# Kernel optimization log

Measured on AMD Instinct MI355X. Metric: run time of the kernel, lower is better.

## Reference

```python
import jax, jax.numpy as jnp
import numpy as np

N_MEL = 80
PRENET = 256
ATT_RNN = 1024
DEC_RNN = 1024
ENC = 512
ATT_DIM = 128
LOC_F = 32
LOC_K = 31


def lstm_cell(x, h, c, wih, whh, bih, bhh):
    # torch LSTMCell gate order: i, f, g, o
    gates = x @ wih.T + bih + h @ whh.T + bhh
    i, f, g, o = jnp.split(gates, 4, axis=-1)
    c_new = jax.nn.sigmoid(f) * c + jax.nn.sigmoid(i) * jnp.tanh(g)
    h_new = jax.nn.sigmoid(o) * jnp.tanh(c_new)
    return h_new, c_new


def setup_inputs() -> dict:
    key = jax.random.key(0)
    ks = jax.random.split(key, 20)
    B, T_IN, T_OUT = 64, 200, 400

    def w(k, shape, fan_in):
        return (jax.random.normal(k, shape, jnp.float32) / np.float32(np.sqrt(fan_in)))

    return {
        "memory": jax.random.normal(ks[0], (B, T_IN, ENC), jnp.float32),
        "decoder_inputs": jax.random.normal(ks[1], (B, N_MEL, T_OUT), jnp.float32),
        "memory_lengths": jax.random.randint(ks[2], (B,), T_IN // 2, T_IN + 1),
        "w_prenet1": w(ks[3], (PRENET, N_MEL), N_MEL),
        "w_prenet2": w(ks[4], (PRENET, PRENET), PRENET),
        "wih_att": w(ks[5], (4 * ATT_RNN, PRENET + ENC), PRENET + ENC),
        "whh_att": w(ks[6], (4 * ATT_RNN, ATT_RNN), ATT_RNN),
        "bih_att": jnp.zeros((4 * ATT_RNN,), jnp.float32),
        "bhh_att": jnp.zeros((4 * ATT_RNN,), jnp.float32),
        "wq": w(ks[7], (ATT_DIM, ATT_RNN), ATT_RNN),
        "wmem": w(ks[8], (ATT_DIM, ENC), ENC),
        "wv": w(ks[9], (1, ATT_DIM), ATT_DIM),
        "wconv": w(ks[10], (LOC_F, 2, LOC_K), 2 * LOC_K),
        "wloc": w(ks[11], (ATT_DIM, LOC_F), LOC_F),
        "wih_dec": w(ks[12], (4 * DEC_RNN, ATT_RNN + ENC), ATT_RNN + ENC),
        "whh_dec": w(ks[13], (4 * DEC_RNN, DEC_RNN), DEC_RNN),
        "bih_dec": jnp.zeros((4 * DEC_RNN,), jnp.float32),
        "bhh_dec": jnp.zeros((4 * DEC_RNN,), jnp.float32),
        "wproj": w(ks[14], (N_MEL, DEC_RNN + ENC), DEC_RNN + ENC),
        "bproj": jnp.zeros((N_MEL,), jnp.float32),
        "wgate": w(ks[15], (1, DEC_RNN + ENC), DEC_RNN + ENC),
        "bgate": jnp.zeros((1,), jnp.float32),
    }


def reference(memory, decoder_inputs, memory_lengths, w_prenet1, w_prenet2,
              wih_att, whh_att, bih_att, bhh_att, wq, wmem, wv, wconv, wloc,
              wih_dec, whh_dec, bih_dec, bhh_dec, wproj, bproj, wgate, bgate):
    B, T_in, _ = memory.shape
    T_out = decoder_inputs.shape[2]

    # parse_decoder_inputs: [B, n_mel, T_out] -> [T_out, B, n_mel]; prepend go frame
    dec_in = jnp.transpose(decoder_inputs, (2, 0, 1))
    dec_in = jnp.concatenate([jnp.zeros((1, B, N_MEL), dec_in.dtype), dec_in], axis=0)

    # PreNet: linear -> relu -> dropout(0.5, training=True always in source)
    dk1, dk2 = jax.random.split(jax.random.key(42))
    x = jax.nn.relu(dec_in @ w_prenet1.T)
    x = jnp.where(jax.random.bernoulli(dk1, 0.5, x.shape), x * 2.0, 0.0)
    x = jax.nn.relu(x @ w_prenet2.T)
    x = jnp.where(jax.random.bernoulli(dk2, 0.5, x.shape), x * 2.0, 0.0)
    x = x[:T_out]  # teacher-forcing inputs, one per decode step

    proc_mem = memory @ wmem.T                                   # [B, T_in, ATT_DIM]
    pad_mask = jnp.arange(T_in)[None, :] >= memory_lengths[:, None]  # True = padded

    def step(carry, x_t):
        att_h, att_c, dec_h, dec_c, aw, awc, ctx = carry
        att_h, att_c = lstm_cell(jnp.concatenate([x_t, ctx], -1), att_h, att_c,
                                 wih_att, whh_att, bih_att, bhh_att)
        # location-sensitive attention
        awcat = jnp.stack([aw, awc], axis=1)                     # [B, 2, T_in]
        loc = jax.lax.conv_general_dilated(
            awcat, wconv, (1,), [(LOC_K // 2, LOC_K // 2)],
            dimension_numbers=("NCH", "OIH", "NCH"))             # [B, LOC_F, T_in]
        proc_loc = jnp.einsum("bft,df->btd", loc, wloc)          # [B, T_in, ATT_DIM]
        pq = att_h @ wq.T                                        # [B, ATT_DIM]
        e = jnp.tanh(proc_mem + pq[:, None, :] + proc_loc) @ wv[0]  # [B, T_in]
        e = jnp.where(pad_mask, -1e9, e)
        aw_new = jax.nn.softmax(e, axis=1)
        ctx = jnp.einsum("bt,bte->be", aw_new, memory)           # [B, ENC]
        awc = awc + aw_new
        dec_h, dec_c = lstm_cell(jnp.concatenate([att_h, ctx], -1), dec_h, dec_c,
                                 wih_dec, whh_dec, bih_dec, bhh_dec)
        dha = jnp.concatenate([dec_h, ctx], axis=1)              # [B, DEC_RNN+ENC]
        mel = dha @ wproj.T + bproj                              # [B, N_MEL]
        gate = dha @ wgate.T + bgate                             # [B, 1]
        return (att_h, att_c, dec_h, dec_c, aw_new, awc, ctx), (mel, gate[:, 0], aw_new)

    z = jnp.zeros
    init = (z((B, ATT_RNN)), z((B, ATT_RNN)), z((B, DEC_RNN)), z((B, DEC_RNN)),
            z((B, T_in)), z((B, T_in)), z((B, ENC)))
    _, (mels, gates, aligns) = jax.lax.scan(step, init, x)
    mel_outputs = jnp.transpose(mels, (1, 2, 0))    # [B, n_mel, T_out]
    gate_outputs = jnp.transpose(gates, (1, 0))     # [B, T_out]
    alignments = jnp.transpose(aligns, (1, 0, 2))   # [B, T_out, T_in]
    return mel_outputs, gate_outputs, alignments
```

## Files before the change

kernel.cpp:

```cpp
#include <hip/hip_runtime.h>
#include <hip/hip_bf16.h>
#include <stdint.h>
#include <stddef.h>

#define SPLIT_MODE 0
#define BITS_MODE  0
#define KSPLIT 16

#define B_    64
#define TIN   200
#define TOUT  400
#define ENC   512
#define NMEL  80
#define PRE   256
#define RNN   1024
#define G4    4096
#define ATTD  128
#define LOCF  32
#define LOCK  31
#define MSIZE 6569984u

__host__ __device__ inline void tf2x32(uint32_t k0, uint32_t k1, uint32_t x0, uint32_t x1,
                                       uint32_t* o0, uint32_t* o1) {
  uint32_t k2 = k0 ^ k1 ^ 0x1BD11BDAu;
#define TFROT(v, r) (((v) << (r)) | ((v) >> (32 - (r))))
#define TFR(r) { x0 += x1; x1 = TFROT(x1, r); x1 ^= x0; }
  x0 += k0; x1 += k1;
  TFR(13) TFR(15) TFR(26) TFR(6)  x0 += k1; x1 += k2 + 1u;
  TFR(17) TFR(29) TFR(16) TFR(24) x0 += k2; x1 += k0 + 2u;
  TFR(13) TFR(15) TFR(26) TFR(6)  x0 += k0; x1 += k1 + 3u;
  TFR(17) TFR(29) TFR(16) TFR(24) x0 += k1; x1 += k2 + 4u;
  TFR(13) TFR(15) TFR(26) TFR(6)  x0 += k2; x1 += k0 + 5u;
  *o0 = x0; *o1 = x1;
#undef TFR
#undef TFROT
}

__device__ inline bool tf_keep(uint32_t ka, uint32_t kb, uint32_t idx) {
#if BITS_MODE == 0
  uint32_t a, b; tf2x32(ka, kb, 0u, idx, &a, &b);
  return (((a ^ b) >> 31) == 0u);
#else
  const uint32_t HALF = MSIZE / 2u;
  uint32_t a, b;
  if (idx < HALF) { tf2x32(ka, kb, idx, idx + HALF, &a, &b); return ((a >> 31) == 0u); }
  else            { tf2x32(ka, kb, idx - HALF, idx, &a, &b); return ((b >> 31) == 0u); }
#endif
}

__device__ inline float sigf(float x) { return 1.f / (1.f + __expf(-x)); }

static const size_t OFF_PM   = 0;
static const size_t OFF_XS   = OFF_PM   + (size_t)B_ * TIN * ATTD;
static const size_t OFF_HATT = OFF_XS   + (size_t)B_ * PRE;
static const size_t OFF_CATT = OFF_HATT + (size_t)B_ * RNN;
static const size_t OFF_HDEC = OFF_CATT + (size_t)B_ * RNN;
static const size_t OFF_CDEC = OFF_HDEC + (size_t)B_ * RNN;
static const size_t OFF_CTX  = OFF_CDEC + (size_t)B_ * RNN;
static const size_t OFF_AW   = OFF_CTX  + (size_t)B_ * ENC;
static const size_t OFF_AWC  = OFF_AW   + (size_t)B_ * TIN;
static const size_t OFF_PART = OFF_AWC  + (size_t)B_ * TIN;

__global__ __launch_bounds__(256) void k_init(float* s, int n) {
  int i = blockIdx.x * 256 + threadIdx.x;
  if (i < n) s[i] = 0.f;
}

__global__ __launch_bounds__(128) void k_procmem(const float* __restrict__ memory,
    const float* __restrict__ wmem, float* __restrict__ pm) {
  int b = blockIdx.x / TIN, tt = blockIdx.x % TIN;
  int d = threadIdx.x;
  __shared__ __align__(16) float m_s[ENC];
  for (int k = d; k < ENC; k += 128) m_s[k] = memory[((size_t)b * TIN + tt) * ENC + k];
  __syncthreads();
  float a = 0.f;
  const float4* w4 = (const float4*)(wmem + (size_t)d * ENC);
  const float4* m4 = (const float4*)m_s;
  #pragma unroll 8
  for (int k = 0; k < ENC / 4; ++k) {
    float4 w = w4[k], v = m4[k];
    a += w.x * v.x + w.y * v.y + w.z * v.z + w.w * v.w;
  }
  pm[((size_t)b * TIN + tt) * ATTD + d] = a;
}

#define WSTR 132
__global__ __launch_bounds__(256) void k_gates(
    const float* __restrict__ in1, int L1,
    const float* __restrict__ in2, int L2,
    const float* __restrict__ in3,
    const float* __restrict__ wih, int wihK,
    const float* __restrict__ whh,
    float* __restrict__ part, int nch) {
  int ctile = blockIdx.x;
  int ks = blockIdx.y;
  int tid = threadIdx.x;
  int cg = tid & 31, bg = tid >> 5;
  __shared__ float xin_s[64 * 68];
  __shared__ float w_s[64 * WSTR];
  float acc[8][4];
  #pragma unroll
  for (int i = 0; i < 8; ++i)
    #pragma unroll
    for (int j = 0; j < 4; ++j) acc[i][j] = 0.f;

  int c_begin = (ks * nch) / KSPLIT, c_end = ((ks + 1) * nch) / KSPLIT;
  for (int cc = c_begin; cc < c_end; ++cc) {
    int k0 = cc * 64;
    const float* src; int sl, so;
    if (k0 < L1)            { src = in1; sl = L1;   so = k0; }
    else if (k0 < L1 + L2)  { src = in2; sl = L2;   so = k0 - L1; }
    else                    { src = in3; sl = 1024; so = k0 - L1 - L2; }
    const float* wsrc; int wl, wo;
    if (k0 < wihK) { wsrc = wih; wl = wihK; wo = k0; }
    else           { wsrc = whh; wl = 1024; wo = k0 - wihK; }

    __syncthreads();
    #pragma unroll
    for (int i = 0; i < 16; ++i) {
      int idx = tid + 256 * i;
      int b = idx >> 6, kk = idx & 63;
      xin_s[kk * 68 + b] = src[(size_t)b * sl + so + kk];
    }
    #pragma unroll
    for (int i = 0; i < 8; ++i) {
      int idx = tid + 256 * i;
      int c = idx >> 4, kq = idx & 15;
      float4 w = *(const float4*)&wsrc[(size_t)(ctile * 128 + c) * wl + wo + kq * 4];
      w_s[(kq * 4 + 0) * WSTR + c] = w.x;
      w_s[(kq * 4 + 1) * WSTR + c] = w.y;
      w_s[(kq * 4 + 2) * WSTR + c] = w.z;
      w_s[(kq * 4 + 3) * WSTR + c] = w.w;
    }
    __syncthreads();
    #pragma unroll 4
    for (int kk = 0; kk < 64; ++kk) {
      float4 w  = *(const float4*)&w_s[kk * WSTR + cg * 4];
      float4 x0 = *(const float4*)&xin_s[kk * 68 + bg * 8];
      float4 x1 = *(const float4*)&xin_s[kk * 68 + bg * 8 + 4];
      float xr[8] = {x0.x, x0.y, x0.z, x0.w, x1.x, x1.y, x1.z, x1.w};
      float wr[4] = {w.x, w.y, w.z, w.w};
      #pragma unroll
      for (int i = 0; i < 8; ++i)
        #pragma unroll
        for (int j = 0; j < 4; ++j) acc[i][j] += xr[i] * wr[j];
    }
  }
  #pragma unroll
  for (int i = 0; i < 8; ++i) {
    float* dst = part + ((size_t)ks * B_ + (bg * 8 + i)) * G4 + ctile * 128 + cg * 4;
    *(float4*)dst = make_float4(acc[i][0], acc[i][1], acc[i][2], acc[i][3]);
  }
}

__global__ __launch_bounds__(512) void k_attention(
    const float* __restrict__ part, float* __restrict__ hatt, float* __restrict__ catt,
    float* __restrict__ aw, float* __restrict__ awc, float* __restrict__ ctx,
    const float* __restrict__ pm, const float* __restrict__ memory,
    const float* __restrict__ wq, const float* __restrict__ wv,
    const float* __restrict__ wconv, const float* __restrict__ wloc,
    const float* __restrict__ bih, const float* __restrict__ bhh,
    const int* __restrict__ memlen, float* __restrict__ out_align, int t) {
  int b = blockIdx.x, tid = threadIdx.x;
  __shared__ float h_s[RNN];
  __shared__ float aw_s[TIN], awc_s[TIN];
  __shared__ float loc_s[LOCF * TIN];
  __shared__ float pq_s[ATTD];
  __shared__ float e4_s[4 * TIN];
  __shared__ float red[512];
  __shared__ float wl_s[ATTD * LOCF];
  __shared__ float wc_s[LOCF * 2 * LOCK];

  for (int k = tid; k < ATTD * LOCF; k += 512) wl_s[k] = wloc[k];
  for (int k = tid; k < LOCF * 2 * LOCK; k += 512) wc_s[k] = wconv[k];

  #pragma unroll
  for (int r = 0; r < 2; ++r) {
    int j = tid + 512 * r;
    float ig = bih[j] + bhh[j];
    float fg = bih[RNN + j] + bhh[RNN + j];
    float gg = bih[2 * RNN + j] + bhh[2 * RNN + j];
    float og = bih[3 * RNN + j] + bhh[3 * RNN + j];
    #pragma unroll
    for (int ks = 0; ks < KSPLIT; ++ks) {
      const float* pr = part + ((size_t)ks * B_ + b) * G4;
      ig += pr[j]; fg += pr[RNN + j]; gg += pr[2 * RNN + j]; og += pr[3 * RNN + j];
    }
    float c = sigf(fg) * catt[(size_t)b * RNN + j] + sigf(ig) * tanhf(gg);
    float h = sigf(og) * tanhf(c);
    catt[(size_t)b * RNN + j] = c;
    hatt[(size_t)b * RNN + j] = h;
    h_s[j] = h;
  }
  for (int k = tid; k < TIN; k += 512) { aw_s[k] = aw[(size_t)b * TIN + k]; awc_s[k] = awc[(size_t)b * TIN + k]; }
  __syncthreads();

  {
    int d = tid & 127, hf = tid >> 7;
    float a = 0.f;
    const float* wr = wq + (size_t)d * RNN + hf * 256;
    const float* hr = h_s + hf * 256;
    #pragma unroll 8
    for (int k = 0; k < 256; ++k) a += hr[k] * wr[k];
    red[tid] = a;
  }
  __syncthreads();
  if (tid < ATTD) pq_s[tid] = red[tid] + red[tid + 128] + red[tid + 256] + red[tid + 384];

  for (int task = tid; task < LOCF * TIN; task += 512) {
    int f = task / TIN, tt = task % TIN;
    float a = 0.f;
    #pragma unroll
    for (int k = 0; k < LOCK; ++k) {
      int s = tt + k - 15;
      if (s >= 0 && s < TIN)
        a += aw_s[s] * wc_s[f * (2 * LOCK) + k] + awc_s[s] * wc_s[f * (2 * LOCK) + LOCK + k];
    }
    loc_s[task] = a;
  }
  __syncthreads();

  for (int task = tid; task < 4 * TIN; task += 512) {
    int hf = task / TIN, tt = task - hf * TIN;
    float acc = 0.f;
    const float* pmr = pm + ((size_t)b * TIN + tt) * ATTD;
    #pragma unroll 4
    for (int d = hf * 32; d < hf * 32 + 32; ++d) {
      float pl = 0.f;
      #pragma unroll
      for (int f = 0; f < LOCF; ++f) pl += loc_s[f * TIN + tt] * wl_s[d * LOCF + f];
      acc += tanhf(pmr[d] + pq_s[d] + pl) * wv[d];
    }
    e4_s[task] = acc;
  }
  __syncthreads();

  int len = memlen[b];
  float ev = -3.0e38f;
  if (tid < TIN)
    ev = (tid < len) ? (e4_s[tid] + e4_s[TIN + tid] + e4_s[2 * TIN + tid] + e4_s[3 * TIN + tid])
                     : -1.0e9f;
  red[tid] = ev;
  __syncthreads();
  for (int s = 256; s > 0; s >>= 1) { if (tid < s) red[tid] = fmaxf(red[tid], red[tid + s]); __syncthreads(); }
  float m = red[0];
  __syncthreads();
  float p = (tid < TIN) ? __expf(ev - m) : 0.f;
  red[tid] = p;
  __syncthreads();
  for (int s = 256; s > 0; s >>= 1) { if (tid < s) red[tid] += red[tid + s]; __syncthreads(); }
  float inv = 1.f / red[0];
  __syncthreads();
  if (tid < TIN) {
    float a = p * inv;
    aw[(size_t)b * TIN + tid] = a;
    awc[(size_t)b * TIN + tid] = awc_s[tid] + a;
    out_align[((size_t)b * TOUT + t) * TIN + tid] = a;
    aw_s[tid] = a;
  }
  __syncthreads();

  {
    float a = 0.f;
    const float* mr = memory + (size_t)b * TIN * ENC + tid;
    #pragma unroll 8
    for (int tt = 0; tt < TIN; ++tt) a += aw_s[tt] * mr[(size_t)tt * ENC];
    ctx[(size_t)b * ENC + tid] = a;
  }
}

__global__ __launch_bounds__(512) void k_outphase(
    const float* __restrict__ part, const float* __restrict__ ctx,
    float* __restrict__ hdec, float* __restrict__ cdec,
    const float* __restrict__ bih, const float* __restrict__ bhh,
    const float* __restrict__ wproj, const float* __restrict__ bproj,
    const float* __restrict__ wgate, const float* __restrict__ bgate,
    float* __restrict__ out,
    const float* __restrict__ dec, const float* __restrict__ w1,
    const float* __restrict__ w2, float* __restrict__ xs,
    uint32_t k1a, uint32_t k1b, uint32_t k2a, uint32_t k2b, int t) {
  int b = blockIdx.x, tid = threadIdx.x;
  __shared__ float dha_s[RNN + ENC];
  __shared__ float red[512];
  __shared__ __align__(16) float in_s[NMEL];
  __shared__ __align__(16) float h2_s[PRE];
  #pragma unroll
  for (int r = 0; r < 2; ++r) {
    int j = tid + 512 * r;
    float ig = bih[j] + bhh[j];
    float fg = bih[RNN + j] + bhh[RNN + j];
    float gg = bih[2 * RNN + j] + bhh[2 * RNN + j];
    float og = bih[3 * RNN + j] + bhh[3 * RNN + j];
    #pragma unroll
    for (int ks = 0; ks < KSPLIT; ++ks) {
      const float* pr = part + ((size_t)ks * B_ + b) * G4;
      ig += pr[j]; fg += pr[RNN + j]; gg += pr[2 * RNN + j]; og += pr[3 * RNN + j];
    }
    float c = sigf(fg) * cdec[(size_t)b * RNN + j] + sigf(ig) * tanhf(gg);
    float h = sigf(og) * tanhf(c);
    cdec[(size_t)b * RNN + j] = c;
    hdec[(size_t)b * RNN + j] = h;
    dha_s[j] = h;
  }
  for (int k = tid; k < ENC; k += 512) dha_s[RNN + k] = ctx[(size_t)b * ENC + k];
  if (t + 1 < TOUT && tid < NMEL)
    in_s[tid] = dec[((size_t)b * NMEL + tid) * TOUT + t];
  __syncthreads();
  float mp = 0.f;
  if (tid < 4 * NMEL) {
    int m = tid % NMEL, hf = tid / NMEL;
    const float* wr = wproj + (size_t)m * (RNN + ENC) + hf * 384;
    const float* dr = dha_s + hf * 384;
    #pragma unroll 8
    for (int k = 0; k < 384; ++k) mp += dr[k] * wr[k];
  }
  red[tid] = mp;
  __syncthreads();
  if (tid < NMEL) {
    float mel = red[tid] + red[tid + NMEL] + red[tid + 2 * NMEL] + red[tid + 3 * NMEL] + bproj[tid];
    out[((size_t)b * NMEL + tid) * TOUT + t] = mel;
  }
  __syncthreads();
  float g = 0.f;
  for (int k = tid; k < RNN + ENC; k += 512) g += dha_s[k] * wgate[k];
  red[tid] = g;
  __syncthreads();
  for (int s = 256; s > 0; s >>= 1) { if (tid < s) red[tid] += red[tid + s]; __syncthreads(); }
  if (tid == 0) out[(size_t)2048000 + (size_t)b * TOUT + t] = red[0] + bgate[0];

  if (t + 1 < TOUT) {
    int tn = t + 1;
    if (tid < PRE) {
      float a = 0.f;
      const float4* w14 = (const float4*)(w1 + (size_t)tid * NMEL);
      const float4* i4  = (const float4*)in_s;
      #pragma unroll
      for (int k = 0; k < NMEL / 4; ++k) {
        float4 w = w14[k], v = i4[k];
        a += w.x * v.x + w.y * v.y + w.z * v.z + w.w * v.w;
      }
      a = fmaxf(a, 0.f);
      uint32_t idx = (uint32_t)((tn * 64 + b) * 256 + tid);
      a = tf_keep(k1a, k1b, idx) ? a * 2.f : 0.f;
      h2_s[tid] = a;
    }
    __syncthreads();
    if (tid < PRE) {
      float a2 = 0.f;
      const float4* w24 = (const float4*)(w2 + (size_t)tid * PRE);
      const float4* h4  = (const float4*)h2_s;
      #pragma unroll 8
      for (int k = 0; k < PRE / 4; ++k) {
        float4 w = w24[k], v = h4[k];
        a2 += w.x * v.x + w.y * v.y + w.z * v.z + w.w * v.w;
      }
      a2 = fmaxf(a2, 0.f);
      uint32_t idx = (uint32_t)((tn * 64 + b) * 256 + tid);
      a2 = tf_keep(k2a, k2b, idx) ? a2 * 2.f : 0.f;
      xs[((size_t)b << 8) + tid] = a2;
    }
  }
}

extern "C" void kernel_launch(void* const* d_in, const int* in_sizes, int n_in,
                              void* d_out, int out_size, void* d_ws, size_t ws_size,
                              hipStream_t stream) {
  (void)in_sizes; (void)n_in; (void)out_size; (void)ws_size;
  const float* memory  = (const float*)d_in[0];
  const float* dec     = (const float*)d_in[1];
  const int*   mlen    = (const int*)d_in[2];
  const float* w1      = (const float*)d_in[3];
  const float* w2      = (const float*)d_in[4];
  const float* wih_att = (const float*)d_in[5];
  const float* whh_att = (const float*)d_in[6];
  const float* bih_att = (const float*)d_in[7];
  const float* bhh_att = (const float*)d_in[8];
  const float* wq      = (const float*)d_in[9];
  const float* wmem    = (const float*)d_in[10];
  const float* wv      = (const float*)d_in[11];
  const float* wconv   = (const float*)d_in[12];
  const float* wloc    = (const float*)d_in[13];
  const float* wih_dec = (const float*)d_in[14];
  const float* whh_dec = (const float*)d_in[15];
  const float* bih_dec = (const float*)d_in[16];
  const float* bhh_dec = (const float*)d_in[17];
  const float* wproj   = (const float*)d_in[18];
  const float* bproj   = (const float*)d_in[19];
  const float* wgate   = (const float*)d_in[20];
  const float* bgate   = (const float*)d_in[21];
  float* out = (float*)d_out;
  float* ws  = (float*)d_ws;

  uint32_t dk1a, dk1b, dk2a, dk2b;
#if SPLIT_MODE == 0
  tf2x32(0u, 42u, 0u, 0u, &dk1a, &dk1b);
  tf2x32(0u, 42u, 0u, 1u, &dk2a, &dk2b);
#else
  uint32_t a0, b0, a1, b1;
  tf2x32(0u, 42u, 0u, 2u, &a0, &b0);
  tf2x32(0u, 42u, 1u, 3u, &a1, &b1);
  dk1a = a0; dk1b = a1; dk2a = b0; dk2b = b1;
#endif

  float* pm   = ws + OFF_PM;
  float* xs   = ws + OFF_XS;
  float* hatt = ws + OFF_HATT; float* catt = ws + OFF_CATT;
  float* hdec = ws + OFF_HDEC; float* cdec = ws + OFF_CDEC;
  float* ctxp = ws + OFF_CTX;
  float* aw   = ws + OFF_AW;   float* awc  = ws + OFF_AWC;
  float* part = ws + OFF_PART;

  int nstate = B_ * (PRE + 4 * RNN + ENC + 2 * TIN);
  k_init<<<(nstate + 255) / 256, 256, 0, stream>>>(xs, nstate);
  k_procmem<<<B_ * TIN, 128, 0, stream>>>(memory, wmem, pm);

  float* out_align = out + 2073600;
  for (int t = 0; t < TOUT; ++t) {
    k_gates<<<dim3(32, KSPLIT), 256, 0, stream>>>(xs, PRE, ctxp, ENC, hatt,
                                                  wih_att, PRE + ENC, whh_att,
                                                  part, 28);
    k_attention<<<B_, 512, 0, stream>>>(part, hatt, catt, aw, awc, ctxp, pm, memory,
                                        wq, wv, wconv, wloc, bih_att, bhh_att,
                                        mlen, out_align, t);
    k_gates<<<dim3(32, KSPLIT), 256, 0, stream>>>(hatt, RNN, ctxp, ENC, hdec,
                                                  wih_dec, RNN + ENC, whh_dec,
                                                  part, 40);
    k_outphase<<<B_, 512, 0, stream>>>(part, ctxp, hdec, cdec, bih_dec, bhh_dec,
                                       wproj, bproj, wgate, bgate, out,
                                       dec, w1, w2, xs, dk1a, dk1b, dk2a, dk2b, t);
  }
}
```

Measured before the change: 68.45 ms.

## Fuse per-timestep kernels into one persistent cooperative kernel with grid syncs

Replaces the four kernel launches per decoder step (1600 in total) with a single cooperative kernel. It loops over all timesteps and separates the gate GEMM, attention, second gate GEMM and output phases with grid-wide syncs. The gate GEMM is remapped to 256 blocks of 512 threads with a K-split of 8 and smaller per-thread tiles. Shared memory becomes a union covering every phase. The aim is to remove launch gaps and per-launch overhead. In exchange, attention and output phases still use only 64 of 256 blocks, grid barriers carry their own cost, and the GEMM tiling changes.

```diff
diff --git a/kernel.cpp b/kernel.cpp
--- a/kernel.cpp
+++ b/kernel.cpp
@@ -1,11 +1,12 @@
 #include <hip/hip_runtime.h>
 #include <hip/hip_bf16.h>
+#include <hip/hip_cooperative_groups.h>
 #include <stdint.h>
 #include <stddef.h>
 
 #define SPLIT_MODE 0
 #define BITS_MODE  0
-#define KSPLIT 16
+#define KSPLIT 8
 
 #define B_    64
 #define TIN   200
@@ -19,6 +20,9 @@
 #define LOCF  32
 #define LOCK  31
 #define MSIZE 6569984u
+#define WSTR  132
+
+namespace cg = cooperative_groups;
 
 __host__ __device__ inline void tf2x32(uint32_t k0, uint32_t k1, uint32_t x0, uint32_t x1,
                                        uint32_t* o0, uint32_t* o1) {
@@ -61,6 +65,27 @@
 static const size_t OFF_AWC  = OFF_AW   + (size_t)B_ * TIN;
 static const size_t OFF_PART = OFF_AWC  + (size_t)B_ * TIN;
 
+union SM {
+  struct { float xin[64 * 68]; float w[64 * WSTR]; } g;
+  struct {
+    float h[RNN]; float awp[TIN]; float awcp[TIN]; float loc[LOCF * TIN];
+    float pq[ATTD]; float e4[4 * TIN]; float red[512];
+    float wl[ATTD * LOCF]; float wc[LOCF * 2 * LOCK];
+  } a;
+  struct { float dha[RNN + ENC]; float red[512]; float inm[NMEL]; float h2[PRE]; } o;
+};
+
+struct Params {
+  const float *memory, *dec, *w1, *w2;
+  const float *wih_att, *whh_att, *bih_att, *bhh_att;
+  const float *wq, *wv, *wconv, *wloc;
+  const float *wih_dec, *whh_dec, *bih_dec, *bhh_dec;
+  const float *wproj, *bproj, *wgate, *bgate;
+  const int* mlen;
+  float *out, *out_align, *pm, *xs, *hatt, *catt, *hdec, *cdec, *ctx, *aw, *awc, *part;
+  uint32_t k1a, k1b, k2a, k2b;
+};
+
 __global__ __launch_bounds__(256) void k_init(float* s, int n) {
   int i = blockIdx.x * 256 + threadIdx.x;
   if (i < n) s[i] = 0.f;
@@ -84,27 +109,18 @@
   pm[((size_t)b * TIN + tt) * ATTD + d] = a;
 }
 
-#define WSTR 132
-__global__ __launch_bounds__(256) void k_gates(
-    const float* __restrict__ in1, int L1,
-    const float* __restrict__ in2, int L2,
-    const float* __restrict__ in3,
-    const float* __restrict__ wih, int wihK,
-    const float* __restrict__ whh,
-    float* __restrict__ part, int nch) {
-  int ctile = blockIdx.x;
-  int ks = blockIdx.y;
-  int tid = threadIdx.x;
+__device__ void gates_phase(SM* sm, const float* in1, int L1, const float* in2, int L2,
+    const float* in3, const float* wih, int wihK, const float* whh,
+    float* part, int nch, int bid, int tid) {
+  int ctile = bid & 31, ks = bid >> 5;
   int cg = tid & 31, bg = tid >> 5;
-  __shared__ float xin_s[64 * 68];
-  __shared__ float w_s[64 * WSTR];
-  float acc[8][4];
+  float acc[4][4];
   #pragma unroll
-  for (int i = 0; i < 8; ++i)
+  for (int i = 0; i < 4; ++i)
     #pragma unroll
     for (int j = 0; j < 4; ++j) acc[i][j] = 0.f;
 
-  int c_begin = (ks * nch) / KSPLIT, c_end = ((ks + 1) * nch) / KSPLIT;
+  int c_begin = (ks * nch) >> 3, c_end = ((ks + 1) * nch) >> 3;
   for (int cc = c_begin; cc < c_end; ++cc) {
     int k0 = cc * 64;
     const float* src; int sl, so;
@@ -117,95 +133,81 @@
 
     __syncthreads();
     #pragma unroll
-    for (int i = 0; i < 16; ++i) {
-      int idx = tid + 256 * i;
+    for (int i = 0; i < 8; ++i) {
+      int idx = tid + 512 * i;
       int b = idx >> 6, kk = idx & 63;
-      xin_s[kk * 68 + b] = src[(size_t)b * sl + so + kk];
-    }
-    #pragma unroll
-    for (int i = 0; i < 8; ++i) {
-      int idx = tid + 256 * i;
+      sm->g.xin[kk * 68 + b] = src[(size_t)b * sl + so + kk];
+    }
+    #pragma unroll
+    for (int i = 0; i < 4; ++i) {
+      int idx = tid + 512 * i;
       int c = idx >> 4, kq = idx & 15;
       float4 w = *(const float4*)&wsrc[(size_t)(ctile * 128 + c) * wl + wo + kq * 4];
-      w_s[(kq * 4 + 0) * WSTR + c] = w.x;
-      w_s[(kq * 4 + 1) * WSTR + c] = w.y;
-      w_s[(kq * 4 + 2) * WSTR + c] = w.z;
-      w_s[(kq * 4 + 3) * WSTR + c] = w.w;
+      sm->g.w[(kq * 4 + 0) * WSTR + c] = w.x;
+      sm->g.w[(kq * 4 + 1) * WSTR + c] = w.y;
+      sm->g.w[(kq * 4 + 2) * WSTR + c] = w.z;
+      sm->g.w[(kq * 4 + 3) * WSTR + c] = w.w;
     }
     __syncthreads();
     #pragma unroll 4
     for (int kk = 0; kk < 64; ++kk) {
-      float4 w  = *(const float4*)&w_s[kk * WSTR + cg * 4];
-      float4 x0 = *(const float4*)&xin_s[kk * 68 + bg * 8];
-      float4 x1 = *(const float4*)&xin_s[kk * 68 + bg * 8 + 4];
-      float xr[8] = {x0.x, x0.y, x0.z, x0.w, x1.x, x1.y, x1.z, x1.w};
+      float4 w = *(const float4*)&sm->g.w[kk * WSTR + cg * 4];
+      float4 x = *(const float4*)&sm->g.xin[kk * 68 + bg * 4];
+      float xr[4] = {x.x, x.y, x.z, x.w};
       float wr[4] = {w.x, w.y, w.z, w.w};
       #pragma unroll
-      for (int i = 0; i < 8; ++i)
+      for (int i = 0; i < 4; ++i)
         #pragma unroll
         for (int j = 0; j < 4; ++j) acc[i][j] += xr[i] * wr[j];
     }
   }
   #pragma unroll
-  for (int i = 0; i < 8; ++i) {
-    float* dst = part + ((size_t)ks * B_ + (bg * 8 + i)) * G4 + ctile * 128 + cg * 4;
+  for (int i = 0; i < 4; ++i) {
+    float* dst = part + ((size_t)ks * B_ + (bg * 4 + i)) * G4 + ctile * 128 + cg * 4;
     *(float4*)dst = make_float4(acc[i][0], acc[i][1], acc[i][2], acc[i][3]);
   }
 }
 
-__global__ __launch_bounds__(512) void k_attention(
-    const float* __restrict__ part, float* __restrict__ hatt, float* __restrict__ catt,
-    float* __restrict__ aw, float* __restrict__ awc, float* __restrict__ ctx,
-    const float* __restrict__ pm, const float* __restrict__ memory,
-    const float* __restrict__ wq, const float* __restrict__ wv,
-    const float* __restrict__ wconv, const float* __restrict__ wloc,
-    const float* __restrict__ bih, const float* __restrict__ bhh,
-    const int* __restrict__ memlen, float* __restrict__ out_align, int t) {
-  int b = blockIdx.x, tid = threadIdx.x;
-  __shared__ float h_s[RNN];
-  __shared__ float aw_s[TIN], awc_s[TIN];
-  __shared__ float loc_s[LOCF * TIN];
-  __shared__ float pq_s[ATTD];
-  __shared__ float e4_s[4 * TIN];
-  __shared__ float red[512];
-  __shared__ float wl_s[ATTD * LOCF];
-  __shared__ float wc_s[LOCF * 2 * LOCK];
-
-  for (int k = tid; k < ATTD * LOCF; k += 512) wl_s[k] = wloc[k];
-  for (int k = tid; k < LOCF * 2 * LOCK; k += 512) wc_s[k] = wconv[k];
+__device__ void attention_phase(SM* sm, const Params& p, int b, int tid, int t) {
+  for (int k = tid; k < ATTD * LOCF; k += 512) sm->a.wl[k] = p.wloc[k];
+  for (int k = tid; k < LOCF * 2 * LOCK; k += 512) sm->a.wc[k] = p.wconv[k];
 
   #pragma unroll
   for (int r = 0; r < 2; ++r) {
     int j = tid + 512 * r;
-    float ig = bih[j] + bhh[j];
-    float fg = bih[RNN + j] + bhh[RNN + j];
-    float gg = bih[2 * RNN + j] + bhh[2 * RNN + j];
-    float og = bih[3 * RNN + j] + bhh[3 * RNN + j];
+    float ig = p.bih_att[j] + p.bhh_att[j];
+    float fg = p.bih_att[RNN + j] + p.bhh_att[RNN + j];
+    float gg = p.bih_att[2 * RNN + j] + p.bhh_att[2 * RNN + j];
+    float og = p.bih_att[3 * RNN + j] + p.bhh_att[3 * RNN + j];
     #pragma unroll
     for (int ks = 0; ks < KSPLIT; ++ks) {
-      const float* pr = part + ((size_t)ks * B_ + b) * G4;
+      const float* pr = p.part + ((size_t)ks * B_ + b) * G4;
       ig += pr[j]; fg += pr[RNN + j]; gg += pr[2 * RNN + j]; og += pr[3 * RNN + j];
     }
-    float c = sigf(fg) * catt[(size_t)b * RNN + j] + sigf(ig) * tanhf(gg);
+    float c = sigf(fg) * p.catt[(size_t)b * RNN + j] + sigf(ig) * tanhf(gg);
     float h = sigf(og) * tanhf(c);
-    catt[(size_t)b * RNN + j] = c;
-    hatt[(size_t)b * RNN + j] = h;
-    h_s[j] = h;
-  }
-  for (int k = tid; k < TIN; k += 512) { aw_s[k] = aw[(size_t)b * TIN + k]; awc_s[k] = awc[(size_t)b * TIN + k]; }
+    p.catt[(size_t)b * RNN + j] = c;
+    p.hatt[(size_t)b * RNN + j] = h;
+    sm->a.h[j] = h;
+  }
+  for (int k = tid; k < TIN; k += 512) {
+    sm->a.awp[k] = p.aw[(size_t)b * TIN + k];
+    sm->a.awcp[k] = p.awc[(size_t)b * TIN + k];
+  }
   __syncthreads();
 
   {
     int d = tid & 127, hf = tid >> 7;
     float a = 0.f;
-    const float* wr = wq + (size_t)d * RNN + hf * 256;
-    const float* hr = h_s + hf * 256;
+    const float* wr = p.wq + (size_t)d * RNN + hf * 256;
+    const float* hr = sm->a.h + hf * 256;
     #pragma unroll 8
     for (int k = 0; k < 256; ++k) a += hr[k] * wr[k];
-    red[tid] = a;
-  }
-  __syncthreads();
-  if (tid < ATTD) pq_s[tid] = red[tid] + red[tid + 128] + red[tid + 256] + red[tid + 384];
+    sm->a.red[tid] = a;
+  }
+  __syncthreads();
+  if (tid < ATTD)
+    sm->a.pq[tid] = sm->a.red[tid] + sm->a.red[tid + 128] + sm->a.red[tid + 256] + sm->a.red[tid + 384];
 
   for (int task = tid; task < LOCF * TIN; task += 512) {
     int f = task / TIN, tt = task % TIN;
@@ -214,126 +216,123 @@
     for (int k = 0; k < LOCK; ++k) {
       int s = tt + k - 15;
       if (s >= 0 && s < TIN)
-        a += aw_s[s] * wc_s[f * (2 * LOCK) + k] + awc_s[s] * wc_s[f * (2 * LOCK) + LOCK + k];
-    }
-    loc_s[task] = a;
+        a += sm->a.awp[s] * sm->a.wc[f * (2 * LOCK) + k] + sm->a.awcp[s] * sm->a.wc[f * (2 * LOCK) + LOCK + k];
+    }
+    sm->a.loc[task] = a;
   }
   __syncthreads();
 
   for (int task = tid; task < 4 * TIN; task += 512) {
     int hf = task / TIN, tt = task - hf * TIN;
     float acc = 0.f;
-    const float* pmr = pm + ((size_t)b * TIN + tt) * ATTD;
+    const float* pmr = p.pm + ((size_t)b * TIN + tt) * ATTD;
     #pragma unroll 4
     for (int d = hf * 32; d < hf * 32 + 32; ++d) {
       float pl = 0.f;
       #pragma unroll
-      for (int f = 0; f < LOCF; ++f) pl += loc_s[f * TIN + tt] * wl_s[d * LOCF + f];
-      acc += tanhf(pmr[d] + pq_s[d] + pl) * wv[d];
-    }
-    e4_s[task] = acc;
-  }
-  __syncthreads();
-
-  int len = memlen[b];
+      for (int f = 0; f < LOCF; ++f) pl += sm->a.loc[f * TIN + tt] * sm->a.wl[d * LOCF + f];
+      acc += tanhf(pmr[d] + sm->a.pq[d] + pl) * p.wv[d];
+    }
+    sm->a.e4[task] = acc;
+  }
+  __syncthreads();
+
+  int len = p.mlen[b];
   float ev = -3.0e38f;
   if (tid < TIN)
-    ev = (tid < len) ? (e4_s[tid] + e4_s[TIN + tid] + e4_s[2 * TIN + tid] + e4_s[3 * TIN + tid])
+    ev = (tid < len) ? (sm->a.e4[tid] + sm->a.e4[TIN + tid] + sm->a.e4[2 * TIN + tid] + sm->a.e4[3 * TIN + tid])
                      : -1.0e9f;
-  red[tid] = ev;
-  __syncthreads();
-  for (int s = 256; s > 0; s >>= 1) { if (tid < s) red[tid] = fmaxf(red[tid], red[tid + s]); __syncthreads(); }
-  float m = red[0];
-  __syncthreads();
-  float p = (tid < TIN) ? __expf(ev - m) : 0.f;
-  red[tid] = p;
-  __syncthreads();
-  for (int s = 256; s > 0; s >>= 1) { if (tid < s) red[tid] += red[tid + s]; __syncthreads(); }
-  float inv = 1.f / red[0];
+  sm->a.red[tid] = ev;
+  __syncthreads();
+  for (int s = 256; s > 0; s >>= 1) {
+    if (tid < s) sm->a.red[tid] = fmaxf(sm->a.red[tid], sm->a.red[tid + s]);
+    __syncthreads();
+  }
+  float m = sm->a.red[0];
+  __syncthreads();
+  float pr = (tid < TIN) ? __expf(ev - m) : 0.f;
+  sm->a.red[tid] = pr;
+  __syncthreads();
+  for (int s = 256; s > 0; s >>= 1) {
+    if (tid < s) sm->a.red[tid] += sm->a.red[tid + s];
+    __syncthreads();
+  }
+  float inv = 1.f / sm->a.red[0];
   __syncthreads();
   if (tid < TIN) {
-    float a = p * inv;
-    aw[(size_t)b * TIN + tid] = a;
-    awc[(size_t)b * TIN + tid] = awc_s[tid] + a;
-    out_align[((size_t)b * TOUT + t) * TIN + tid] = a;
-    aw_s[tid] = a;
+    float a = pr * inv;
+    p.aw[(size_t)b * TIN + tid] = a;
+    p.awc[(size_t)b * TIN + tid] = sm->a.awcp[tid] + a;
+    p.out_align[((size_t)b * TOUT + t) * TIN + tid] = a;
+    sm->a.awp[tid] = a;
   }
   __syncthreads();
 
   {
     float a = 0.f;
-    const float* mr = memory + (size_t)b * TIN * ENC + tid;
+    const float* mr = p.memory + (size_t)b * TIN * ENC + tid;
     #pragma unroll 8
-    for (int tt = 0; tt < TIN; ++tt) a += aw_s[tt] * mr[(size_t)tt * ENC];
-    ctx[(size_t)b * ENC + tid] = a;
-  }
-}
-
-__global__ __launch_bounds__(512) void k_outphase(
-    const float* __restrict__ part, const float* __restrict__ ctx,
-    float* __restrict__ hdec, float* __restrict__ cdec,
-    const float* __restrict__ bih, const float* __restrict__ bhh,
-    const float* __restrict__ wproj, const float* __restrict__ bproj,
-    const float* __restrict__ wgate, const float* __restrict__ bgate,
-    float* __restrict__ out,
-    const float* __restrict__ dec, const float* __restrict__ w1,
-    const float* __restrict__ w2, float* __restrict__ xs,
-    uint32_t k1a, uint32_t k1b, uint32_t k2a, uint32_t k2b, int t) {
-  int b = blockIdx.x, tid = threadIdx.x;
-  __shared__ float dha_s[RNN + ENC];
-  __shared__ float red[512];
-  __shared__ __align__(16) float in_s[NMEL];
-  __shared__ __align__(16) float h2_s[PRE];
+    for (int tt = 0; tt < TIN; ++tt) a += sm->a.awp[tt] * mr[(size_t)tt * ENC];
+    p.ctx[(size_t)b * ENC + tid] = a;
+  }
+}
+
+__device__ void outphase_phase(SM* sm, const Params& p, int b, int tid, int t) {
   #pragma unroll
   for (int r = 0; r < 2; ++r) {
     int j = tid + 512 * r;
-    float ig = bih[j] + bhh[j];
-    float fg = bih[RNN + j] + bhh[RNN + j];
-    float gg = bih[2 * RNN + j] + bhh[2 * RNN + j];
-    float og = bih[3 * RNN + j] + bhh[3 * RNN + j];
+    float ig = p.bih_dec[j] + p.bhh_dec[j];
+    float fg = p.bih_dec[RNN + j] + p.bhh_dec[RNN + j];
+    float gg = p.bih_dec[2 * RNN + j] + p.bhh_dec[2 * RNN + j];
+    float og = p.bih_dec[3 * RNN + j] + p.bhh_dec[3 * RNN + j];
     #pragma unroll
     for (int ks = 0; ks < KSPLIT; ++ks) {
-      const float* pr = part + ((size_t)ks * B_ + b) * G4;
+      const float* pr = p.part + ((size_t)ks * B_ + b) * G4;
       ig += pr[j]; fg += pr[RNN + j]; gg += pr[2 * RNN + j]; og += pr[3 * RNN + j];
     }
-    float c = sigf(fg) * cdec[(size_t)b * RNN + j] + sigf(ig) * tanhf(gg);
+    float c = sigf(fg) * p.cdec[(size_t)b * RNN + j] + sigf(ig) * tanhf(gg);
     float h = sigf(og) * tanhf(c);
-    cdec[(size_t)b * RNN + j] = c;
-    hdec[(size_t)b * RNN + j] = h;
-    dha_s[j] = h;
-  }
-  for (int k = tid; k < ENC; k += 512) dha_s[RNN + k] = ctx[(size_t)b * ENC + k];
+    p.cdec[(size_t)b * RNN + j] = c;
+    p.hdec[(size_t)b * RNN + j] = h;
+    sm->o.dha[j] = h;
+  }
+  for (int k = tid; k < ENC; k += 512) sm->o.dha[RNN + k] = p.ctx[(size_t)b * ENC + k];
   if (t + 1 < TOUT && tid < NMEL)
-    in_s[tid] = dec[((size_t)b * NMEL + tid) * TOUT + t];
-  __syncthreads();
+    sm->o.inm[tid] = p.dec[((size_t)b * NMEL + tid) * TOUT + t];
+  __syncthreads();
+
   float mp = 0.f;
   if (tid < 4 * NMEL) {
     int m = tid % NMEL, hf = tid / NMEL;
-    const float* wr = wproj + (size_t)m * (RNN + ENC) + hf * 384;
-    const float* dr = dha_s + hf * 384;
+    const float* wr = p.wproj + (size_t)m * (RNN + ENC) + hf * 384;
+    const float* dr = sm->o.dha + hf * 384;
     #pragma unroll 8
     for (int k = 0; k < 384; ++k) mp += dr[k] * wr[k];
   }
-  red[tid] = mp;
+  sm->o.red[tid] = mp;
   __syncthreads();
   if (tid < NMEL) {
-    float mel = red[tid] + red[tid + NMEL] + red[tid + 2 * NMEL] + red[tid + 3 * NMEL] + bproj[tid];
-    out[((size_t)b * NMEL + tid) * TOUT + t] = mel;
+    float mel = sm->o.red[tid] + sm->o.red[tid + NMEL] + sm->o.red[tid + 2 * NMEL]
+              + sm->o.red[tid + 3 * NMEL] + p.bproj[tid];
+    p.out[((size_t)b * NMEL + tid) * TOUT + t] = mel;
   }
   __syncthreads();
   float g = 0.f;
-  for (int k = tid; k < RNN + ENC; k += 512) g += dha_s[k] * wgate[k];
-  red[tid] = g;
-  __syncthreads();
-  for (int s = 256; s > 0; s >>= 1) { if (tid < s) red[tid] += red[tid + s]; __syncthreads(); }
-  if (tid == 0) out[(size_t)2048000 + (size_t)b * TOUT + t] = red[0] + bgate[0];
+  for (int k = tid; k < RNN + ENC; k += 512) g += sm->o.dha[k] * p.wgate[k];
+  sm->o.red[tid] = g;
+  __syncthreads();
+  for (int s = 256; s > 0; s >>= 1) {
+    if (tid < s) sm->o.red[tid] += sm->o.red[tid + s];
+    __syncthreads();
+  }
+  if (tid == 0) p.out[(size_t)2048000 + (size_t)b * TOUT + t] = sm->o.red[0] + p.bgate[0];
 
   if (t + 1 < TOUT) {
     int tn = t + 1;
     if (tid < PRE) {
       float a = 0.f;
-      const float4* w14 = (const float4*)(w1 + (size_t)tid * NMEL);
-      const float4* i4  = (const float4*)in_s;
+      const float4* w14 = (const float4*)(p.w1 + (size_t)tid * NMEL);
+      const float4* i4  = (const float4*)sm->o.inm;
       #pragma unroll
       for (int k = 0; k < NMEL / 4; ++k) {
         float4 w = w14[k], v = i4[k];
@@ -341,14 +340,14 @@
       }
       a = fmaxf(a, 0.f);
       uint32_t idx = (uint32_t)((tn * 64 + b) * 256 + tid);
-      a = tf_keep(k1a, k1b, idx) ? a * 2.f : 0.f;
-      h2_s[tid] = a;
+      a = tf_keep(p.k1a, p.k1b, idx) ? a * 2.f : 0.f;
+      sm->o.h2[tid] = a;
     }
     __syncthreads();
     if (tid < PRE) {
       float a2 = 0.f;
-      const float4* w24 = (const float4*)(w2 + (size_t)tid * PRE);
-      const float4* h4  = (const float4*)h2_s;
+      const float4* w24 = (const float4*)(p.w2 + (size_t)tid * PRE);
+      const float4* h4  = (const float4*)sm->o.h2;
       #pragma unroll 8
       for (int k = 0; k < PRE / 4; ++k) {
         float4 w = w24[k], v = h4[k];
@@ -356,9 +355,35 @@
       }
       a2 = fmaxf(a2, 0.f);
       uint32_t idx = (uint32_t)((tn * 64 + b) * 256 + tid);
-      a2 = tf_keep(k2a, k2b, idx) ? a2 * 2.f : 0.f;
-      xs[((size_t)b << 8) + tid] = a2;
-    }
+      a2 = tf_keep(p.k2a, p.k2b, idx) ? a2 * 2.f : 0.f;
+      p.xs[((size_t)b << 8) + tid] = a2;
+    }
+  }
+}
+
+__global__ __launch_bounds__(512) void k_persist(Params p) {
+  cg::grid_group grid = cg::this_grid();
+  int bid = blockIdx.x, tid = threadIdx.x;
+  __shared__ __align__(16) SM sm;
+
+  for (int t = 0; t < TOUT; ++t) {
+    gates_phase(&sm, p.xs, PRE, p.ctx, ENC, p.hatt, p.wih_att, PRE + ENC, p.whh_att,
+                p.part, 28, bid, tid);
+    __threadfence();
+    grid.sync();
+
+    if (bid < B_) attention_phase(&sm, p, bid, tid, t);
+    __threadfence();
+    grid.sync();
+
+    gates_phase(&sm, p.hatt, RNN, p.ctx, ENC, p.hdec, p.wih_dec, RNN + ENC, p.whh_dec,
+                p.part, 40, bid, tid);
+    __threadfence();
+    grid.sync();
+
+    if (bid < B_) outphase_phase(&sm, p, bid, tid, t);
+    __threadfence();
+    grid.sync();
   }
 }
 
@@ -414,19 +439,18 @@
   k_init<<<(nstate + 255) / 256, 256, 0, stream>>>(xs, nstate);
   k_procmem<<<B_ * TIN, 128, 0, stream>>>(memory, wmem, pm);
 
-  float* out_align = out + 2073600;
-  for (int t = 0; t < TOUT; ++t) {
-    k_gates<<<dim3(32, KSPLIT), 256, 0, stream>>>(xs, PRE, ctxp, ENC, hatt,
-                                                  wih_att, PRE + ENC, whh_att,
-                                                  part, 28);
-    k_attention<<<B_, 512, 0, stream>>>(part, hatt, catt, aw, awc, ctxp, pm, memory,
-                                        wq, wv, wconv, wloc, bih_att, bhh_att,
-                                        mlen, out_align, t);
-    k_gates<<<dim3(32, KSPLIT), 256, 0, stream>>>(hatt, RNN, ctxp, ENC, hdec,
-                                                  wih_dec, RNN + ENC, whh_dec,
-                                                  part, 40);
-    k_outphase<<<B_, 512, 0, stream>>>(part, ctxp, hdec, cdec, bih_dec, bhh_dec,
-                                       wproj, bproj, wgate, bgate, out,
-                                       dec, w1, w2, xs, dk1a, dk1b, dk2a, dk2b, t);
-  }
-}
+  Params p;
+  p.memory = memory; p.dec = dec; p.w1 = w1; p.w2 = w2;
+  p.wih_att = wih_att; p.whh_att = whh_att; p.bih_att = bih_att; p.bhh_att = bhh_att;
+  p.wq = wq; p.wv = wv; p.wconv = wconv; p.wloc = wloc;
+  p.wih_dec = wih_dec; p.whh_dec = whh_dec; p.bih_dec = bih_dec; p.bhh_dec = bhh_dec;
+  p.wproj = wproj; p.bproj = bproj; p.wgate = wgate; p.bgate = bgate;
+  p.mlen = mlen;
+  p.out = out; p.out_align = out + 2073600;
+  p.pm = pm; p.xs = xs; p.hatt = hatt; p.catt = catt; p.hdec = hdec; p.cdec = cdec;
+  p.ctx = ctxp; p.aw = aw; p.awc = awc; p.part = part;
+  p.k1a = dk1a; p.k1b = dk1b; p.k2a = dk2a; p.k2b = dk2b;
+
+  void* args[] = { &p };
+  hipLaunchCooperativeKernel((const void*)k_persist, dim3(256), dim3(512), args, 0, stream);
+}
```

Measured after the change: 210.6 ms. 208% more time.
